# Kernel tuning notes

Hardware: AMD Instinct MI355X
Metric: run time of the kernel (lower is better)

## Reference

```python
import jax, jax.numpy as jnp
import numpy as np

HID = 768
INTER = 3072
H = 12
DH = 64
N = 16384
W = 256   # attention_width
L = 512   # per-sequence length (power of 2, used via the uint32 bit-mask trick)


def rotate_every_two(x):
    x1 = x[..., ::2]
    x2 = x[..., 1::2]
    return jnp.stack((-x2, x1), axis=-1).reshape(x.shape)


def setup_inputs() -> dict:
    key = jax.random.key(0)
    ks = jax.random.split(key, 6)
    # GPT-J style interleaved rotary tables: sin/cos each value repeated twice
    inv_freq = 1.0 / (10000.0 ** (np.arange(0, DH, 2) / DH))  # [DH/2]
    ang = np.arange(N)[:, None] * inv_freq[None, :]           # [N, DH/2]
    pos_sin = jnp.asarray(np.repeat(np.sin(ang), 2, axis=-1), dtype=jnp.float32)
    pos_cos = jnp.asarray(np.repeat(np.cos(ang), 2, axis=-1), dtype=jnp.float32)
    return {
        "x": jax.random.normal(ks[0], (N, HID), dtype=jnp.float32),
        "normed_ages": jax.random.normal(ks[1], (N,), dtype=jnp.float32),
        "pos_sin": pos_sin,
        "pos_cos": pos_cos,
        "ln_scale": jnp.ones((HID,), dtype=jnp.float32),
        "ln_offset": jnp.zeros((HID,), dtype=jnp.float32),
        "w_in": jax.random.normal(ks[2], (HID, 3 * HID + INTER), dtype=jnp.float32) * 0.02,
        "b_in": jnp.zeros((3 * HID + INTER,), dtype=jnp.float32),
        "w_out": jax.random.normal(ks[3], (HID + INTER, HID), dtype=jnp.float32) * 0.02,
        "b_out": jnp.zeros((HID,), dtype=jnp.float32),
        "length": L,
    }


def reference(x, normed_ages, pos_sin, pos_cos, ln_scale, ln_offset,
              w_in, b_in, w_out, b_out, length):
    # LayerNorm (haiku: eps=1e-5, create_scale/offset)
    mu = jnp.mean(x, axis=-1, keepdims=True)
    var = jnp.var(x, axis=-1, keepdims=True)
    xn = (x - mu) * jax.lax.rsqrt(var + 1e-5) * ln_scale + ln_offset

    # fused QKV + FF projection (note: original computes x_with_ages but never uses it)
    mid = xn @ w_in + b_in
    q, k, v, ff = jnp.split(mid, [HID, 2 * HID, 3 * HID], axis=-1)

    def to_heads(t):  # [N, HID] -> [H, N, DH]
        return t.reshape(N, H, DH).transpose(1, 0, 2)

    q, k, v = to_heads(q), to_heads(k), to_heads(v)

    # rotary ('per_head'): sincos broadcast over heads
    sin, cos = pos_sin[None], pos_cos[None]
    q = q * cos + rotate_every_two(q) * sin
    k = k * cos + rotate_every_two(k) * sin

    # local (sliding-window, causal, within-sequence) attention, chunked by W
    C = W
    nc = N // C
    qc = q.reshape(H, nc, C, DH)
    kc = k.reshape(H, nc, C, DH)
    vc = v.reshape(H, nc, C, DH)
    kprev = jnp.concatenate([jnp.zeros_like(kc[:, :1]), kc[:, :-1]], axis=1)
    vprev = jnp.concatenate([jnp.zeros_like(vc[:, :1]), vc[:, :-1]], axis=1)
    kcat = jnp.concatenate([kprev, kc], axis=2)  # [H, nc, 2C, DH]
    vcat = jnp.concatenate([vprev, vc], axis=2)

    qi = (jnp.arange(nc) * C)[:, None] + jnp.arange(C)        # [nc, C]
    kj = (jnp.arange(nc) * C)[:, None] - C + jnp.arange(2 * C)  # [nc, 2C]
    lm = ~(jnp.uint32(length) - jnp.uint32(1))  # same bit-trick as the module
    same_seq = ((qi[:, :, None].astype(jnp.uint32) & lm) ==
                (jnp.maximum(kj, 0)[:, None, :].astype(jnp.uint32) & lm))
    d = qi[:, :, None] - kj[:, None, :]
    mask = (kj[:, None, :] >= 0) & (d >= 0) & (d < W) & same_seq  # [nc, C, 2C]

    scale = 1.0 / jnp.sqrt(jnp.float32(DH))
    scores = jnp.einsum('hncd,hnkd->hnck', qc, kcat) * scale
    scores = jnp.where(mask[None], scores, jnp.float32(-1e30))
    probs = jax.nn.softmax(scores, axis=-1)
    attn = jnp.einsum('hnck,hnkd->hncd', probs, vcat)

    attn = attn.reshape(H, N, DH).transpose(1, 0, 2).reshape(N, HID)
    combined = jnp.concatenate([attn, jax.nn.gelu(ff)], axis=-1)
    return xn + combined @ w_out + b_out
```

## Files before the change

### kernel.cpp

```cpp
#include <hip/hip_runtime.h>

#define N_TOK 16384
#define HIDN  768
#define MIDN  5376
#define COMBN 3840
#define NH    12
#define DHD   64
#define CHUNK 256
#define WIN   256

typedef short s16x8 __attribute__((ext_vector_type(8)));
typedef short s16x4 __attribute__((ext_vector_type(4)));
typedef float f32x4 __attribute__((ext_vector_type(4)));

__device__ __forceinline__ float bf2f(unsigned short u){
  union { unsigned u; float f; } x; x.u = ((unsigned)u) << 16; return x.f;
}
__device__ __forceinline__ unsigned short f2bf(float f){
  union { float f; unsigned u; } x; x.f = f;
  unsigned r = x.u + 0x7fffu + ((x.u >> 16) & 1u);
  return (unsigned short)(r >> 16);
}
__device__ __forceinline__ float gelu_fast(float x){
  float u = -1.5957691216057308f * (x + 0.044715f * x * x * x);
  return x / (1.f + __expf(u));
}
__device__ __forceinline__ void glds16(const void* g, void* l){
  __builtin_amdgcn_global_load_lds(
      (const __attribute__((address_space(1))) unsigned*)g,
      (__attribute__((address_space(3))) unsigned*)l, 16, 0, 0);
}

__global__ __launch_bounds__(256) void transpose_f2b(
    const float* __restrict__ in, unsigned short* __restrict__ out,
    int R, int Cc)
{
  __shared__ short t[64 * 72];
  const int tid = threadIdx.x;
  const int r0 = blockIdx.y * 64, c0 = blockIdx.x * 64;
  #pragma unroll
  for (int rep = 0; rep < 4; rep++){
    int v = tid + 256 * rep;
    int r = v >> 4, s = v & 15;
    float4 d = *(const float4*)(in + (size_t)(r0 + r) * Cc + c0 + s * 4);
    s16x4 o = { (short)f2bf(d.x), (short)f2bf(d.y), (short)f2bf(d.z), (short)f2bf(d.w) };
    *(s16x4*)(t + r * 72 + s * 4) = o;
  }
  __syncthreads();
  #pragma unroll
  for (int rep = 0; rep < 2; rep++){
    int v = tid + 256 * rep;
    int c = v & 63, s2 = v >> 6;
    s16x8 d;
    #pragma unroll
    for (int j = 0; j < 8; j++) d[j] = t[(s2 * 8 + j) * 72 + c];
    *(s16x8*)(out + (size_t)(c0 + c) * R + r0 + s2 * 8) = d;
  }
}

__global__ __launch_bounds__(256) void ln_kernel(
    const float* __restrict__ x, const float* __restrict__ sc,
    const float* __restrict__ ofs, unsigned short* __restrict__ xn)
{
  const int lane = threadIdx.x & 63, wv = threadIdx.x >> 6;
  const int row = blockIdx.x * 4 + wv;
  const float4* xr = (const float4*)(x + (size_t)row * HIDN);
  float4 vals[3];
  float sum = 0.f, sq = 0.f;
  #pragma unroll
  for (int j = 0; j < 3; j++){
    vals[j] = xr[lane + 64 * j];
    sum += vals[j].x + vals[j].y + vals[j].z + vals[j].w;
    sq  += vals[j].x * vals[j].x + vals[j].y * vals[j].y
         + vals[j].z * vals[j].z + vals[j].w * vals[j].w;
  }
  #pragma unroll
  for (int o = 1; o < 64; o <<= 1){ sum += __shfl_xor(sum, o); sq += __shfl_xor(sq, o); }
  const float mu = sum * (1.f / HIDN);
  const float rs = rsqrtf(fmaxf(sq * (1.f / HIDN) - mu * mu, 0.f) + 1e-5f);
  s16x4* xo = (s16x4*)(xn + (size_t)row * HIDN);
  const float4* scp = (const float4*)sc;
  const float4* ofp = (const float4*)ofs;
  #pragma unroll
  for (int j = 0; j < 3; j++){
    int p = lane + 64 * j;
    float4 s = scp[p], o = ofp[p];
    s16x4 w;
    w[0] = (short)f2bf((vals[j].x - mu) * rs * s.x + o.x);
    w[1] = (short)f2bf((vals[j].y - mu) * rs * s.y + o.y);
    w[2] = (short)f2bf((vals[j].z - mu) * rs * s.z + o.z);
    w[3] = (short)f2bf((vals[j].w - mu) * rs * s.w + o.w);
    xo[p] = w;
  }
}

template<int K>
__device__ __forceinline__ void gemm_pipe(
    const unsigned short* __restrict__ A, const unsigned short* __restrict__ BT,
    short* AsBuf, short* BsBuf,
    int tid, int quad, int l15, int wr, int wc, int m0, int n0,
    f32x4 acc[8][4])
{
  constexpr int T = K / 32;
  constexpr int BUFSZ = 256 * 32;

  const int srow = tid >> 2;
  const int ksw  = ((tid & 3) ^ ((tid >> 3) & 3)) * 8;
  const unsigned short* Ap = A  + (size_t)(m0 + srow) * K + ksw;
  const unsigned short* Bp = BT + (size_t)(n0 + srow) * K + ksw;
  const size_t halfstep = (size_t)128 * K;

  auto stage = [&](int tt){
    char* Ad = ((char*)(AsBuf + (size_t)(tt & 3) * BUFSZ)) + tid * 16;
    char* Bd = ((char*)(BsBuf + (size_t)(tt & 3) * BUFSZ)) + tid * 16;
    const unsigned short* Asrc = Ap + tt * 32;
    const unsigned short* Bsrc = Bp + tt * 32;
    glds16(Asrc,            Ad);
    glds16(Asrc + halfstep, Ad + 8192);
    glds16(Bsrc,            Bd);
    glds16(Bsrc + halfstep, Bd + 8192);
  };

  const int seg = ((quad ^ ((l15 >> 1) & 3)) << 4);
  int offA[8], offB[4];
  #pragma unroll
  for (int mf = 0; mf < 8; mf++) offA[mf] = (wr * 128 + mf * 16 + l15) * 64 + seg;
  #pragma unroll
  for (int nf = 0; nf < 4; nf++) offB[nf] = (wc * 64 + nf * 16 + l15) * 64 + seg;

  stage(0); stage(1);
  asm volatile("s_waitcnt vmcnt(4)" ::: "memory");
  asm volatile("s_barrier" ::: "memory");

  s16x8 a[4], a2[4], b[4];
  {
    const char* A0 = (const char*)AsBuf;
    const char* B0 = (const char*)BsBuf;
    #pragma unroll
    for (int i = 0; i < 4; i++) a[i] = *(const s16x8*)(A0 + offA[i]);
    #pragma unroll
    for (int j = 0; j < 4; j++) b[j] = *(const s16x8*)(B0 + offB[j]);
  }

  #pragma unroll 4
  for (int t = 0; t < T; t++){
    if (t + 2 < T) stage(t + 2);
    const char* Ab = (const char*)(AsBuf + (size_t)(t & 3) * BUFSZ);
    #pragma unroll
    for (int i = 0; i < 4; i++) a2[i] = *(const s16x8*)(Ab + offA[4 + i]);
    __builtin_amdgcn_s_setprio(1);
    #pragma unroll
    for (int i = 0; i < 4; i++)
      #pragma unroll
      for (int j = 0; j < 4; j++)
        acc[i][j] = __builtin_amdgcn_mfma_f32_16x16x32_bf16(a[i], b[j], acc[i][j], 0, 0, 0);
    #pragma unroll
    for (int i = 0; i < 4; i++)
      #pragma unroll
      for (int j = 0; j < 4; j++)
        acc[4 + i][j] = __builtin_amdgcn_mfma_f32_16x16x32_bf16(a2[i], b[j], acc[4 + i][j], 0, 0, 0);
    __builtin_amdgcn_s_setprio(0);
    if (t + 1 < T){
      if (t + 2 < T){ asm volatile("s_waitcnt vmcnt(4)" ::: "memory"); }
      else          { asm volatile("s_waitcnt vmcnt(0)" ::: "memory"); }
      asm volatile("s_barrier" ::: "memory");
      const char* An = (const char*)(AsBuf + (size_t)((t + 1) & 3) * BUFSZ);
      const char* Bn = (const char*)(BsBuf + (size_t)((t + 1) & 3) * BUFSZ);
      #pragma unroll
      for (int i = 0; i < 4; i++) a[i] = *(const s16x8*)(An + offA[i]);
      #pragma unroll
      for (int j = 0; j < 4; j++) b[j] = *(const s16x8*)(Bn + offB[j]);
    }
  }
}

__global__ __launch_bounds__(512, 2) void gemm1_k(
    const unsigned short* __restrict__ A, const unsigned short* __restrict__ BT,
    const float* __restrict__ bias,
    unsigned short* __restrict__ qb, unsigned short* __restrict__ kb,
    unsigned short* __restrict__ vb, unsigned short* __restrict__ comb)
{
  __shared__ short As[4][256 * 32];
  __shared__ short Bs[4][256 * 32];
  const int tid = threadIdx.x, lane = tid & 63, wv = tid >> 6;
  const int quad = lane >> 4, l15 = lane & 15;
  const int wr = wv >> 2, wc = wv & 3;
  const int n0 = blockIdx.x * 256, m0 = blockIdx.y * 256;

  f32x4 acc[8][4];
  #pragma unroll
  for (int i = 0; i < 8; i++)
    #pragma unroll
    for (int j = 0; j < 4; j++) acc[i][j] = (f32x4){0.f,0.f,0.f,0.f};

  gemm_pipe<HIDN>(A, BT, &As[0][0], &Bs[0][0], tid, quad, l15, wr, wc, m0, n0, acc);

  unsigned short* dstb; int cb; bool isff = false;
  if (n0 < 768)       { dstb = qb;   cb = n0; }
  else if (n0 < 1536) { dstb = kb;   cb = n0 - 768; }
  else if (n0 < 2304) { dstb = vb;   cb = n0 - 1536; }
  else                { dstb = comb; cb = n0 - 1536; isff = true; }
  const int rowstride = isff ? COMBN : HIDN;
  #pragma unroll
  for (int nf = 0; nf < 4; nf++){
    const int colg = n0 + wc * 64 + nf * 16 + l15;
    const float bsv = bias[colg];
    const int col = cb + wc * 64 + nf * 16 + l15;
    #pragma unroll
    for (int mf = 0; mf < 8; mf++){
      #pragma unroll
      for (int r = 0; r < 4; r++){
        const int row = m0 + wr * 128 + mf * 16 + quad * 4 + r;
        float val = acc[mf][nf][r] + bsv;
        if (isff) val = gelu_fast(val);
        dstb[(size_t)row * rowstride + col] = f2bf(val);
      }
    }
  }
}

__global__ __launch_bounds__(512, 2) void gemm2_k(
    const unsigned short* __restrict__ A, const unsigned short* __restrict__ BT,
    const float* __restrict__ bias, const unsigned short* __restrict__ xn,
    float* __restrict__ outp)
{
  __shared__ short As[4][256 * 32];
  __shared__ short Bs[4][256 * 32];
  const int tid = threadIdx.x, lane = tid & 63, wv = tid >> 6;
  const int quad = lane >> 4, l15 = lane & 15;
  const int wr = wv >> 2, wc = wv & 3;
  const int n0 = blockIdx.x * 256, m0 = blockIdx.y * 256;

  f32x4 acc[8][4];
  #pragma unroll
  for (int i = 0; i < 8; i++)
    #pragma unroll
    for (int j = 0; j < 4; j++) acc[i][j] = (f32x4){0.f,0.f,0.f,0.f};

  gemm_pipe<COMBN>(A, BT, &As[0][0], &Bs[0][0], tid, quad, l15, wr, wc, m0, n0, acc);

  #pragma unroll
  for (int nf = 0; nf < 4; nf++){
    const int col = n0 + wc * 64 + nf * 16 + l15;
    const float bsv = bias[col];
    #pragma unroll
    for (int mf = 0; mf < 8; mf++){
      #pragma unroll
      for (int r = 0; r < 4; r++){
        const int row = m0 + wr * 128 + mf * 16 + quad * 4 + r;
        const size_t o = (size_t)row * HIDN + col;
        outp[o] = bf2f(xn[o]) + acc[mf][nf][r] + bsv;
      }
    }
  }
}

__global__ __launch_bounds__(384) void rope_qk(
    unsigned short* __restrict__ qb, unsigned short* __restrict__ kb,
    const float* __restrict__ psin, const float* __restrict__ pcos)
{
  __shared__ float ss[2048], cs[2048];
  const int tid = threadIdx.x, g = blockIdx.x;
  #pragma unroll
  for (int rep = 0; rep < 6; rep++){
    int idx = rep * 384 + tid;
    if (idx < 2048){
      int tok = idx >> 5, p = idx & 31;
      size_t gt = ((size_t)(g * 64 + tok)) * DHD + 2 * p;
      ss[idx] = psin[gt];
      cs[idx] = pcos[gt];
    }
  }
  __syncthreads();
  const int p = tid & 31;
  unsigned* q32 = (unsigned*)qb;
  unsigned* k32 = (unsigned*)kb;
  for (int tok = 0; tok < 64; tok++){
    const size_t a = ((size_t)(g * 64 + tok)) * 384 + tid;
    const float s = ss[tok * 32 + p], c0 = cs[tok * 32 + p];
    unsigned u = q32[a];
    float e = bf2f((unsigned short)(u & 0xffff));
    float d = bf2f((unsigned short)(u >> 16));
    q32[a] = (unsigned)f2bf((e * c0 - d * s) * 0.125f)
           | (((unsigned)f2bf((d * c0 + e * s) * 0.125f)) << 16);
    u = k32[a];
    e = bf2f((unsigned short)(u & 0xffff));
    d = bf2f((unsigned short)(u >> 16));
    k32[a] = (unsigned)f2bf(e * c0 - d * s)
           | (((unsigned)f2bf(d * c0 + e * s)) << 16);
  }
}

__global__ __launch_bounds__(256) void attn_kernel(
    const unsigned short* __restrict__ qb, const unsigned short* __restrict__ kb,
    const unsigned short* __restrict__ vb, unsigned short* __restrict__ comb,
    const int* __restrict__ lenp)
{
  __shared__ short Ks[2][64 * 72];
  __shared__ short Vt[2][64 * 64];
  __shared__ short Ps[4][16 * 72];
  const int tid = threadIdx.x, lane = tid & 63, wv = tid >> 6;
  const int quad = lane >> 4, l15 = lane & 15;
  const int h = blockIdx.y, c = blockIdx.x;
  const unsigned lm = ~((unsigned)lenp[0] - 1u);
  const int i0 = c * CHUNK + wv * 64;
  const unsigned short* qh = qb + h * DHD;
  const unsigned short* kh = kb + h * DHD;
  const unsigned short* vh = vb + h * DHD;

  s16x8 qf[4][2];
  #pragma unroll
  for (int rt = 0; rt < 4; rt++){
    const unsigned short* qr = qh + (size_t)(i0 + rt * 16 + l15) * HIDN;
    qf[rt][0] = *(const s16x8*)(qr + quad * 8);
    qf[rt][1] = *(const s16x8*)(qr + 32 + quad * 8);
  }

  f32x4 O[4][4];
  float mm[4][4], ll[4][4];
  #pragma unroll
  for (int rt = 0; rt < 4; rt++)
    #pragma unroll
    for (int j = 0; j < 4; j++){ O[rt][j] = (f32x4){0,0,0,0}; mm[rt][j] = -1e30f; ll[rt][j] = 0.f; }
  short* myP = &Ps[wv][0];

  const int skey = tid & 63, sseg = tid >> 6;
  const int jb0 = c * CHUNK - 256;
  s16x8 kr[2], vr[2];

  auto issue = [&](int jb){
    if (jb >= 0){
      const unsigned short* kp = kh + (size_t)(jb + skey) * HIDN + sseg * 16;
      const unsigned short* vp = vh + (size_t)(jb + skey) * HIDN + sseg * 16;
      kr[0] = *(const s16x8*)(kp);     kr[1] = *(const s16x8*)(kp + 8);
      vr[0] = *(const s16x8*)(vp);     vr[1] = *(const s16x8*)(vp + 8);
    } else {
      kr[0] = kr[1] = vr[0] = vr[1] = (s16x8){0,0,0,0,0,0,0,0};
    }
  };

  issue(jb0);
  for (int tb = 0; tb < 8; tb++){
    const int jb = jb0 + tb * 64;
    const int buf = tb & 1;
    short* Kb = &Ks[buf][0];
    short* Vb = &Vt[buf][0];
    *(s16x8*)(Kb + skey * 72 + sseg * 16)     = kr[0];
    *(s16x8*)(Kb + skey * 72 + sseg * 16 + 8) = kr[1];
    #pragma unroll
    for (int half = 0; half < 2; half++)
      #pragma unroll
      for (int j = 0; j < 8; j++){
        const int d = sseg * 16 + half * 8 + j;
        Vb[d * 64 + (((skey & 56) ^ ((d & 7) << 3)) | (skey & 7))] = vr[half][j];
      }
    if (tb < 7) issue(jb + 64);
    __syncthreads();

    const bool act = (jb >= 0) && (jb <= i0 + 63) && (jb + 63 >= i0 - 255) &&
                     (((unsigned)i0 & lm) == ((unsigned)jb & lm));
    if (!act) continue;

    #pragma unroll
    for (int rt = 0; rt < 4; rt++){
      const int ilo = i0 + rt * 16;
      if (ilo + 15 < jb || ilo - (jb + 63) >= WIN) continue;
      f32x4 sc[4];
      #pragma unroll
      for (int ct = 0; ct < 4; ct++){
        const short* kbase = Kb + (ct * 16 + l15) * 72 + quad * 8;
        const s16x8 b0 = *(const s16x8*)(kbase);
        const s16x8 b1 = *(const s16x8*)(kbase + 32);
        f32x4 aa = (f32x4){0,0,0,0};
        aa = __builtin_amdgcn_mfma_f32_16x16x32_bf16(qf[rt][0], b0, aa, 0, 0, 0);
        aa = __builtin_amdgcn_mfma_f32_16x16x32_bf16(qf[rt][1], b1, aa, 0, 0, 0);
        sc[ct] = aa;
      }
      float alph[4];
      #pragma unroll
      for (int r = 0; r < 4; r++){
        const int i = ilo + quad * 4 + r;
        #pragma unroll
        for (int ct = 0; ct < 4; ct++){
          const unsigned dd = (unsigned)(i - (jb + ct * 16 + l15));
          if (dd >= 256u) sc[ct][r] = -1e30f;
        }
        float mx = fmaxf(fmaxf(sc[0][r], sc[1][r]), fmaxf(sc[2][r], sc[3][r]));
        mx = fmaxf(mx, __shfl_xor(mx, 1));
        mx = fmaxf(mx, __shfl_xor(mx, 2));
        mx = fmaxf(mx, __shfl_xor(mx, 4));
        mx = fmaxf(mx, __shfl_xor(mx, 8));
        const float mnew = fmaxf(mm[rt][r], mx);
        alph[r] = __expf(mm[rt][r] - mnew);
        mm[rt][r] = mnew;
        float p0 = __expf(sc[0][r] - mnew);
        float p1 = __expf(sc[1][r] - mnew);
        float p2 = __expf(sc[2][r] - mnew);
        float p3 = __expf(sc[3][r] - mnew);
        sc[0][r] = p0; sc[1][r] = p1; sc[2][r] = p2; sc[3][r] = p3;
        float rsum = (p0 + p1) + (p2 + p3);
        rsum += __shfl_xor(rsum, 1);
        rsum += __shfl_xor(rsum, 2);
        rsum += __shfl_xor(rsum, 4);
        rsum += __shfl_xor(rsum, 8);
        ll[rt][r] = ll[rt][r] * alph[r] + rsum;
      }
      #pragma unroll
      for (int co = 0; co < 4; co++)
        #pragma unroll
        for (int r = 0; r < 4; r++) O[rt][co][r] *= alph[r];
      #pragma unroll
      for (int r = 0; r < 4; r++){
        const int prow = quad * 4 + r;
        #pragma unroll
        for (int ct = 0; ct < 4; ct++)
          myP[prow * 72 + ct * 16 + l15] = (short)f2bf(sc[ct][r]);
      }
      #pragma unroll
      for (int ks2 = 0; ks2 < 2; ks2++){
        const s16x8 pf = *(const s16x8*)(myP + l15 * 72 + ks2 * 32 + quad * 8);
        #pragma unroll
        for (int co = 0; co < 4; co++){
          const int d = co * 16 + l15;
          const s16x8 vf = *(const s16x8*)(Vb + d * 64 +
                              ((ks2 * 32 + quad * 8) ^ ((d & 7) << 3)));
          O[rt][co] = __builtin_amdgcn_mfma_f32_16x16x32_bf16(pf, vf, O[rt][co], 0, 0, 0);
        }
      }
    }
  }

  #pragma unroll
  for (int rt = 0; rt < 4; rt++)
    #pragma unroll
    for (int co = 0; co < 4; co++)
      #pragma unroll
      for (int r = 0; r < 4; r++){
        const int tok = i0 + rt * 16 + quad * 4 + r;
        comb[(size_t)tok * COMBN + h * DHD + co * 16 + l15] = f2bf(O[rt][co][r] / ll[rt][r]);
      }
}

extern "C" void kernel_launch(void* const* d_in, const int* in_sizes, int n_in,
                              void* d_out, int out_size, void* d_ws, size_t ws_size,
                              hipStream_t stream)
{
  const float* x     = (const float*)d_in[0];
  const float* psin  = (const float*)d_in[2];
  const float* pcos  = (const float*)d_in[3];
  const float* lns   = (const float*)d_in[4];
  const float* lno   = (const float*)d_in[5];
  const float* w_in  = (const float*)d_in[6];
  const float* b_in  = (const float*)d_in[7];
  const float* w_out = (const float*)d_in[8];
  const float* b_out = (const float*)d_in[9];
  const int*   lenp  = (const int*)d_in[10];
  float* out = (float*)d_out;

  char* ws = (char*)d_ws;
  size_t off = 0;
  unsigned short* xn    = (unsigned short*)(ws + off); off += (size_t)N_TOK * HIDN * 2;
  unsigned short* wInT  = (unsigned short*)(ws + off); off += (size_t)MIDN * HIDN * 2;
  unsigned short* wOutT = (unsigned short*)(ws + off); off += (size_t)HIDN * COMBN * 2;
  unsigned short* qbuf  = (unsigned short*)(ws + off); off += (size_t)N_TOK * HIDN * 2;
  unsigned short* kbuf  = (unsigned short*)(ws + off); off += (size_t)N_TOK * HIDN * 2;
  unsigned short* vbuf  = (unsigned short*)(ws + off); off += (size_t)N_TOK * HIDN * 2;
  unsigned short* comb  = (unsigned short*)(ws + off); off += (size_t)N_TOK * COMBN * 2;

  transpose_f2b<<<dim3(MIDN/64, HIDN/64), 256, 0, stream>>>(w_in, wInT, HIDN, MIDN);
  transpose_f2b<<<dim3(HIDN/64, COMBN/64), 256, 0, stream>>>(w_out, wOutT, COMBN, HIDN);
  ln_kernel<<<dim3(N_TOK/4), 256, 0, stream>>>(x, lns, lno, xn);
  gemm1_k<<<dim3(MIDN/256, N_TOK/256), 512, 0, stream>>>(
      xn, wInT, b_in, qbuf, kbuf, vbuf, comb);
  rope_qk<<<dim3(N_TOK/64), 384, 0, stream>>>(qbuf, kbuf, psin, pcos);
  attn_kernel<<<dim3(N_TOK/CHUNK, NH), 256, 0, stream>>>(
      qbuf, kbuf, vbuf, comb, lenp);
  gemm2_k<<<dim3(HIDN/256, N_TOK/256), 512, 0, stream>>>(
      comb, wOutT, b_out, xn, out);
}
```

Baseline: 715.2 us.

## Deepen GEMM prefetch to three stages, stage epilogue via LDS, swizzle block order

The shared GEMM pipeline now issues global-to-LDS loads three k-steps ahead instead of two, using all four LDS buffers, with the vmcnt waits adjusted to match. The aim is to hide more memory latency behind MFMA work. gemm1 now writes its bf16 output through a swizzled LDS tile and stores full 16-byte rows, replacing scattered 2-byte stores, at the cost of extra syncs and LDS traffic. gemm1, gemm2 and the attention kernel also remap block IDs in an XCD-aware order so that neighbouring tiles share L2 on the same chiplet.

New measurement: 751.8 us. +5.1%, slower.

```diff
diff --git a/kernel.cpp b/kernel.cpp
--- a/kernel.cpp
+++ b/kernel.cpp
@@ -128,8 +128,8 @@
   #pragma unroll
   for (int nf = 0; nf < 4; nf++) offB[nf] = (wc * 64 + nf * 16 + l15) * 64 + seg;
 
-  stage(0); stage(1);
-  asm volatile("s_waitcnt vmcnt(4)" ::: "memory");
+  stage(0); stage(1); stage(2);
+  asm volatile("s_waitcnt vmcnt(8)" ::: "memory");
   asm volatile("s_barrier" ::: "memory");
 
   s16x8 a[4], a2[4], b[4];
@@ -144,7 +144,7 @@
 
   #pragma unroll 4
   for (int t = 0; t < T; t++){
-    if (t + 2 < T) stage(t + 2);
+    if (t + 3 < T) stage(t + 3);
     const char* Ab = (const char*)(AsBuf + (size_t)(t & 3) * BUFSZ);
     #pragma unroll
     for (int i = 0; i < 4; i++) a2[i] = *(const s16x8*)(Ab + offA[4 + i]);
@@ -161,8 +161,9 @@
         acc[4 + i][j] = __builtin_amdgcn_mfma_f32_16x16x32_bf16(a2[i], b[j], acc[4 + i][j], 0, 0, 0);
     __builtin_amdgcn_s_setprio(0);
     if (t + 1 < T){
-      if (t + 2 < T){ asm volatile("s_waitcnt vmcnt(4)" ::: "memory"); }
-      else          { asm volatile("s_waitcnt vmcnt(0)" ::: "memory"); }
+      if (t + 3 < T)      { asm volatile("s_waitcnt vmcnt(8)" ::: "memory"); }
+      else if (t + 2 < T) { asm volatile("s_waitcnt vmcnt(4)" ::: "memory"); }
+      else                { asm volatile("s_waitcnt vmcnt(0)" ::: "memory"); }
       asm volatile("s_barrier" ::: "memory");
       const char* An = (const char*)(AsBuf + (size_t)((t + 1) & 3) * BUFSZ);
       const char* Bn = (const char*)(BsBuf + (size_t)((t + 1) & 3) * BUFSZ);
@@ -180,12 +181,16 @@
     unsigned short* __restrict__ qb, unsigned short* __restrict__ kb,
     unsigned short* __restrict__ vb, unsigned short* __restrict__ comb)
 {
-  __shared__ short As[4][256 * 32];
-  __shared__ short Bs[4][256 * 32];
+  __shared__ short SM[65536];
   const int tid = threadIdx.x, lane = tid & 63, wv = tid >> 6;
   const int quad = lane >> 4, l15 = lane & 15;
   const int wr = wv >> 2, wc = wv & 3;
-  const int n0 = blockIdx.x * 256, m0 = blockIdx.y * 256;
+
+  const int nbx = gridDim.x;
+  const int nwg = nbx * gridDim.y;
+  const int bid = blockIdx.x + blockIdx.y * nbx;
+  const int swzb = (bid & 7) * (nwg >> 3) + (bid >> 3);
+  const int n0 = (swzb % nbx) * 256, m0 = (swzb / nbx) * 256;
 
   f32x4 acc[8][4];
   #pragma unroll
@@ -193,7 +198,7 @@
     #pragma unroll
     for (int j = 0; j < 4; j++) acc[i][j] = (f32x4){0.f,0.f,0.f,0.f};
 
-  gemm_pipe<HIDN>(A, BT, &As[0][0], &Bs[0][0], tid, quad, l15, wr, wc, m0, n0, acc);
+  gemm_pipe<HIDN>(A, BT, &SM[0], &SM[32768], tid, quad, l15, wr, wc, m0, n0, acc);
 
   unsigned short* dstb; int cb; bool isff = false;
   if (n0 < 768)       { dstb = qb;   cb = n0; }
@@ -201,20 +206,34 @@
   else if (n0 < 2304) { dstb = vb;   cb = n0 - 1536; }
   else                { dstb = comb; cb = n0 - 1536; isff = true; }
   const int rowstride = isff ? COMBN : HIDN;
+
+  __syncthreads();
+  short* Cs = &SM[0];
   #pragma unroll
   for (int nf = 0; nf < 4; nf++){
-    const int colg = n0 + wc * 64 + nf * 16 + l15;
-    const float bsv = bias[colg];
-    const int col = cb + wc * 64 + nf * 16 + l15;
+    const int col = wc * 64 + nf * 16 + l15;
+    const float bsv = bias[n0 + col];
     #pragma unroll
     for (int mf = 0; mf < 8; mf++){
       #pragma unroll
       for (int r = 0; r < 4; r++){
-        const int row = m0 + wr * 128 + mf * 16 + quad * 4 + r;
+        const int row = wr * 128 + mf * 16 + quad * 4 + r;
         float val = acc[mf][nf][r] + bsv;
         if (isff) val = gelu_fast(val);
-        dstb[(size_t)row * rowstride + col] = f2bf(val);
-      }
+        const int c8 = (col >> 3) ^ (row & 7);
+        Cs[row * 256 + c8 * 8 + (col & 7)] = f2bf(val);
+      }
+    }
+  }
+  __syncthreads();
+  {
+    const int row = tid >> 1, ch = (tid & 1) * 16;
+    unsigned short* gout = dstb + (size_t)(m0 + row) * rowstride + cb;
+    #pragma unroll
+    for (int k = 0; k < 16; k++){
+      const int c8 = ch + k;
+      s16x8 v = *(const s16x8*)(Cs + row * 256 + ((c8 ^ (row & 7)) * 8));
+      *(s16x8*)(gout + c8 * 8) = v;
     }
   }
 }
@@ -224,12 +243,16 @@
     const float* __restrict__ bias, const unsigned short* __restrict__ xn,
     float* __restrict__ outp)
 {
-  __shared__ short As[4][256 * 32];
-  __shared__ short Bs[4][256 * 32];
+  __shared__ short SM[65536];
   const int tid = threadIdx.x, lane = tid & 63, wv = tid >> 6;
   const int quad = lane >> 4, l15 = lane & 15;
   const int wr = wv >> 2, wc = wv & 3;
-  const int n0 = blockIdx.x * 256, m0 = blockIdx.y * 256;
+
+  const int nbx = gridDim.x;
+  const int nwg = nbx * gridDim.y;
+  const int bid = blockIdx.x + blockIdx.y * nbx;
+  const int swzb = (bid & 7) * (nwg >> 3) + (bid >> 3);
+  const int n0 = (swzb % nbx) * 256, m0 = (swzb / nbx) * 256;
 
   f32x4 acc[8][4];
   #pragma unroll
@@ -237,7 +260,7 @@
     #pragma unroll
     for (int j = 0; j < 4; j++) acc[i][j] = (f32x4){0.f,0.f,0.f,0.f};
 
-  gemm_pipe<COMBN>(A, BT, &As[0][0], &Bs[0][0], tid, quad, l15, wr, wc, m0, n0, acc);
+  gemm_pipe<COMBN>(A, BT, &SM[0], &SM[32768], tid, quad, l15, wr, wc, m0, n0, acc);
 
   #pragma unroll
   for (int nf = 0; nf < 4; nf++){
@@ -301,7 +324,12 @@
   __shared__ short Ps[4][16 * 72];
   const int tid = threadIdx.x, lane = tid & 63, wv = tid >> 6;
   const int quad = lane >> 4, l15 = lane & 15;
-  const int h = blockIdx.y, c = blockIdx.x;
+
+  const int nwg = gridDim.x * gridDim.y;
+  const int bid = blockIdx.x + blockIdx.y * gridDim.x;
+  const int swzb = (bid & 7) * (nwg >> 3) + (bid >> 3);
+  const int c = swzb % gridDim.x, h = swzb / gridDim.x;
+
   const unsigned lm = ~((unsigned)lenp[0] - 1u);
   const int i0 = c * CHUNK + wv * 64;
   const unsigned short* qh = qb + h * DHD;
```

## Replace pipelined 256x256 GEMM tiles with simple 128x128 single-buffer tiles

Applied to the files above, without the earlier changes.

Both GEMMs move from 256x256 tiles with 512 threads and a 4-deep async LDS pipeline to 128x128 tiles with 256 threads and a single shared buffer, synchronised twice per k-step. This cuts LDS use and registers per block so more blocks fit per CU, and gives gemm2 more blocks (768 instead of 192). The cost is lower data reuse per tile and no overlap between global loads and MFMA work.

After: 684.5 us. -4.3%, faster.

```diff
diff --git a/kernel.cpp b/kernel.cpp
--- a/kernel.cpp
+++ b/kernel.cpp
@@ -95,105 +95,68 @@
 }
 
 template<int K>
-__device__ __forceinline__ void gemm_pipe(
+__device__ __forceinline__ void gemm_tile128(
     const unsigned short* __restrict__ A, const unsigned short* __restrict__ BT,
-    short* AsBuf, short* BsBuf,
+    short* As, short* Bs,
     int tid, int quad, int l15, int wr, int wc, int m0, int n0,
-    f32x4 acc[8][4])
+    f32x4 acc[4][4])
 {
   constexpr int T = K / 32;
-  constexpr int BUFSZ = 256 * 32;
-
   const int srow = tid >> 2;
   const int ksw  = ((tid & 3) ^ ((tid >> 3) & 3)) * 8;
   const unsigned short* Ap = A  + (size_t)(m0 + srow) * K + ksw;
   const unsigned short* Bp = BT + (size_t)(n0 + srow) * K + ksw;
-  const size_t halfstep = (size_t)128 * K;
-
-  auto stage = [&](int tt){
-    char* Ad = ((char*)(AsBuf + (size_t)(tt & 3) * BUFSZ)) + tid * 16;
-    char* Bd = ((char*)(BsBuf + (size_t)(tt & 3) * BUFSZ)) + tid * 16;
-    const unsigned short* Asrc = Ap + tt * 32;
-    const unsigned short* Bsrc = Bp + tt * 32;
-    glds16(Asrc,            Ad);
-    glds16(Asrc + halfstep, Ad + 8192);
-    glds16(Bsrc,            Bd);
-    glds16(Bsrc + halfstep, Bd + 8192);
-  };
+  const size_t hstep = (size_t)64 * K;
+  char* Ad = ((char*)As) + tid * 16;
+  char* Bd = ((char*)Bs) + tid * 16;
 
   const int seg = ((quad ^ ((l15 >> 1) & 3)) << 4);
-  int offA[8], offB[4];
-  #pragma unroll
-  for (int mf = 0; mf < 8; mf++) offA[mf] = (wr * 128 + mf * 16 + l15) * 64 + seg;
+  int offA[4], offB[4];
+  #pragma unroll
+  for (int mf = 0; mf < 4; mf++) offA[mf] = (wr * 64 + mf * 16 + l15) * 64 + seg;
   #pragma unroll
   for (int nf = 0; nf < 4; nf++) offB[nf] = (wc * 64 + nf * 16 + l15) * 64 + seg;
 
-  stage(0); stage(1);
-  asm volatile("s_waitcnt vmcnt(4)" ::: "memory");
-  asm volatile("s_barrier" ::: "memory");
-
-  s16x8 a[4], a2[4], b[4];
-  {
-    const char* A0 = (const char*)AsBuf;
-    const char* B0 = (const char*)BsBuf;
-    #pragma unroll
-    for (int i = 0; i < 4; i++) a[i] = *(const s16x8*)(A0 + offA[i]);
-    #pragma unroll
-    for (int j = 0; j < 4; j++) b[j] = *(const s16x8*)(B0 + offB[j]);
-  }
-
-  #pragma unroll 4
   for (int t = 0; t < T; t++){
-    if (t + 2 < T) stage(t + 2);
-    const char* Ab = (const char*)(AsBuf + (size_t)(t & 3) * BUFSZ);
-    #pragma unroll
-    for (int i = 0; i < 4; i++) a2[i] = *(const s16x8*)(Ab + offA[4 + i]);
-    __builtin_amdgcn_s_setprio(1);
+    __syncthreads();
+    glds16(Ap + t * 32,         Ad);
+    glds16(Ap + t * 32 + hstep, Ad + 4096);
+    glds16(Bp + t * 32,         Bd);
+    glds16(Bp + t * 32 + hstep, Bd + 4096);
+    __syncthreads();
+    s16x8 a[4], b[4];
+    #pragma unroll
+    for (int i = 0; i < 4; i++) a[i] = *(const s16x8*)(((const char*)As) + offA[i]);
+    #pragma unroll
+    for (int j = 0; j < 4; j++) b[j] = *(const s16x8*)(((const char*)Bs) + offB[j]);
     #pragma unroll
     for (int i = 0; i < 4; i++)
       #pragma unroll
       for (int j = 0; j < 4; j++)
         acc[i][j] = __builtin_amdgcn_mfma_f32_16x16x32_bf16(a[i], b[j], acc[i][j], 0, 0, 0);
-    #pragma unroll
-    for (int i = 0; i < 4; i++)
-      #pragma unroll
-      for (int j = 0; j < 4; j++)
-        acc[4 + i][j] = __builtin_amdgcn_mfma_f32_16x16x32_bf16(a2[i], b[j], acc[4 + i][j], 0, 0, 0);
-    __builtin_amdgcn_s_setprio(0);
-    if (t + 1 < T){
-      if (t + 2 < T){ asm volatile("s_waitcnt vmcnt(4)" ::: "memory"); }
-      else          { asm volatile("s_waitcnt vmcnt(0)" ::: "memory"); }
-      asm volatile("s_barrier" ::: "memory");
-      const char* An = (const char*)(AsBuf + (size_t)((t + 1) & 3) * BUFSZ);
-      const char* Bn = (const char*)(BsBuf + (size_t)((t + 1) & 3) * BUFSZ);
-      #pragma unroll
-      for (int i = 0; i < 4; i++) a[i] = *(const s16x8*)(An + offA[i]);
-      #pragma unroll
-      for (int j = 0; j < 4; j++) b[j] = *(const s16x8*)(Bn + offB[j]);
-    }
-  }
-}
-
-__global__ __launch_bounds__(512, 2) void gemm1_k(
+  }
+}
+
+__global__ __launch_bounds__(256, 3) void gemm1_k(
     const unsigned short* __restrict__ A, const unsigned short* __restrict__ BT,
     const float* __restrict__ bias,
     unsigned short* __restrict__ qb, unsigned short* __restrict__ kb,
     unsigned short* __restrict__ vb, unsigned short* __restrict__ comb)
 {
-  __shared__ short As[4][256 * 32];
-  __shared__ short Bs[4][256 * 32];
+  __shared__ short As[128 * 32];
+  __shared__ short Bs[128 * 32];
   const int tid = threadIdx.x, lane = tid & 63, wv = tid >> 6;
   const int quad = lane >> 4, l15 = lane & 15;
-  const int wr = wv >> 2, wc = wv & 3;
-  const int n0 = blockIdx.x * 256, m0 = blockIdx.y * 256;
-
-  f32x4 acc[8][4];
-  #pragma unroll
-  for (int i = 0; i < 8; i++)
+  const int wr = wv >> 1, wc = wv & 1;
+  const int n0 = blockIdx.x * 128, m0 = blockIdx.y * 128;
+
+  f32x4 acc[4][4];
+  #pragma unroll
+  for (int i = 0; i < 4; i++)
     #pragma unroll
     for (int j = 0; j < 4; j++) acc[i][j] = (f32x4){0.f,0.f,0.f,0.f};
 
-  gemm_pipe<HIDN>(A, BT, &As[0][0], &Bs[0][0], tid, quad, l15, wr, wc, m0, n0, acc);
+  gemm_tile128<HIDN>(A, BT, As, Bs, tid, quad, l15, wr, wc, m0, n0, acc);
 
   unsigned short* dstb; int cb; bool isff = false;
   if (n0 < 768)       { dstb = qb;   cb = n0; }
@@ -201,16 +164,17 @@
   else if (n0 < 2304) { dstb = vb;   cb = n0 - 1536; }
   else                { dstb = comb; cb = n0 - 1536; isff = true; }
   const int rowstride = isff ? COMBN : HIDN;
+
   #pragma unroll
   for (int nf = 0; nf < 4; nf++){
     const int colg = n0 + wc * 64 + nf * 16 + l15;
     const float bsv = bias[colg];
     const int col = cb + wc * 64 + nf * 16 + l15;
     #pragma unroll
-    for (int mf = 0; mf < 8; mf++){
+    for (int mf = 0; mf < 4; mf++){
       #pragma unroll
       for (int r = 0; r < 4; r++){
-        const int row = m0 + wr * 128 + mf * 16 + quad * 4 + r;
+        const int row = m0 + wr * 64 + mf * 16 + quad * 4 + r;
         float val = acc[mf][nf][r] + bsv;
         if (isff) val = gelu_fast(val);
         dstb[(size_t)row * rowstride + col] = f2bf(val);
@@ -219,35 +183,35 @@
   }
 }
 
-__global__ __launch_bounds__(512, 2) void gemm2_k(
+__global__ __launch_bounds__(256, 3) void gemm2_k(
     const unsigned short* __restrict__ A, const unsigned short* __restrict__ BT,
     const float* __restrict__ bias, const unsigned short* __restrict__ xn,
     float* __restrict__ outp)
 {
-  __shared__ short As[4][256 * 32];
-  __shared__ short Bs[4][256 * 32];
+  __shared__ short As[128 * 32];
+  __shared__ short Bs[128 * 32];
   const int tid = threadIdx.x, lane = tid & 63, wv = tid >> 6;
   const int quad = lane >> 4, l15 = lane & 15;
-  const int wr = wv >> 2, wc = wv & 3;
-  const int n0 = blockIdx.x * 256, m0 = blockIdx.y * 256;
-
-  f32x4 acc[8][4];
-  #pragma unroll
-  for (int i = 0; i < 8; i++)
+  const int wr = wv >> 1, wc = wv & 1;
+  const int n0 = blockIdx.x * 128, m0 = blockIdx.y * 128;
+
+  f32x4 acc[4][4];
+  #pragma unroll
+  for (int i = 0; i < 4; i++)
     #pragma unroll
     for (int j = 0; j < 4; j++) acc[i][j] = (f32x4){0.f,0.f,0.f,0.f};
 
-  gemm_pipe<COMBN>(A, BT, &As[0][0], &Bs[0][0], tid, quad, l15, wr, wc, m0, n0, acc);
+  gemm_tile128<COMBN>(A, BT, As, Bs, tid, quad, l15, wr, wc, m0, n0, acc);
 
   #pragma unroll
   for (int nf = 0; nf < 4; nf++){
     const int col = n0 + wc * 64 + nf * 16 + l15;
     const float bsv = bias[col];
     #pragma unroll
-    for (int mf = 0; mf < 8; mf++){
+    for (int mf = 0; mf < 4; mf++){
       #pragma unroll
       for (int r = 0; r < 4; r++){
-        const int row = m0 + wr * 128 + mf * 16 + quad * 4 + r;
+        const int row = m0 + wr * 64 + mf * 16 + quad * 4 + r;
         const size_t o = (size_t)row * HIDN + col;
         outp[o] = bf2f(xn[o]) + acc[mf][nf][r] + bsv;
       }
@@ -470,11 +434,11 @@
   transpose_f2b<<<dim3(MIDN/64, HIDN/64), 256, 0, stream>>>(w_in, wInT, HIDN, MIDN);
   transpose_f2b<<<dim3(HIDN/64, COMBN/64), 256, 0, stream>>>(w_out, wOutT, COMBN, HIDN);
   ln_kernel<<<dim3(N_TOK/4), 256, 0, stream>>>(x, lns, lno, xn);
-  gemm1_k<<<dim3(MIDN/256, N_TOK/256), 512, 0, stream>>>(
+  gemm1_k<<<dim3(MIDN/128, N_TOK/128), 256, 0, stream>>>(
       xn, wInT, b_in, qbuf, kbuf, vbuf, comb);
   rope_qk<<<dim3(N_TOK/64), 384, 0, stream>>>(qbuf, kbuf, psin, pcos);
   attn_kernel<<<dim3(N_TOK/CHUNK, NH), 256, 0, stream>>>(
       qbuf, kbuf, vbuf, comb, lenp);
-  gemm2_k<<<dim3(HIDN/256, N_TOK/256), 512, 0, stream>>>(
+  gemm2_k<<<dim3(HIDN/128, N_TOK/128), 256, 0, stream>>>(
       comb, wOutT, b_out, xn, out);
 }
```
